# Optimization experiments

Measured on AMD Instinct MI355X. Metric: run time of the kernel, lower is better.

Reference implementation:

```python
import jax, jax.numpy as jnp
import numpy as np
import math

N, S, E, BS = 8, 8192, 256, 8


def setup_inputs() -> dict:
    key = jax.random.key(0)
    k1, k2, k3 = jax.random.split(key, 3)
    seq_vector = jax.random.normal(k1, (N, S, E), dtype=jnp.float32)
    # Conv1d weight [target_dim, source_dim] (kernel size 1 squeezed), default torch init scale
    bound = 1.0 / math.sqrt(E)
    W = jax.random.uniform(k2, (E, E), minval=-bound, maxval=bound, dtype=jnp.float32)
    sigma = math.sqrt(1.0 / (BS * E))
    bias = jax.random.uniform(k3, (BS,), minval=-sigma, maxval=sigma, dtype=jnp.float32)
    return {"seq_vector": seq_vector, "W": W, "bias": bias}


def reference(seq_vector, W, bias):
    n, s, e = seq_vector.shape
    bs = bias.shape[0]
    # 1x1 conv == per-token projection: [N,S,E] x [T,E] -> [N,S,T]
    features = jnp.einsum('nse,te->nst', seq_vector, W)
    # group sequence into blocks: [N, S//bs, bs, T]
    fb = features.reshape(n, s // bs, bs, -1)
    # blockwise causal (strictly lower-triangular) sum == exclusive cumsum over block dim
    excl = jnp.cumsum(fb, axis=2) - fb
    # position i gets bias[i]; position 0 additionally gets bias[0] a second time
    b_eff = bias.at[0].add(bias[0])  # [bs]
    out = excl + b_eff[None, None, :, None]
    return out.reshape(n, s, -1)
```

## Files before the change

### kernel.cpp

```cpp
#include <hip/hip_runtime.h>


typedef short short8 __attribute__((ext_vector_type(8)));
typedef float floatx4 __attribute__((ext_vector_type(4)));
typedef unsigned short ushort4v __attribute__((ext_vector_type(4)));

typedef const __attribute__((address_space(1))) unsigned int* gas_u32p;
typedef __attribute__((address_space(3))) unsigned int* las_u32p;

#define WAIT_VMCNT(n) __builtin_amdgcn_s_waitcnt(0x0F70 | ((n) & 0xF) | ((((n) >> 4) & 0x3) << 14))

__device__ __forceinline__ void gl2lds16(const void* g, void* l) {
    __builtin_amdgcn_global_load_lds((gas_u32p)g, (las_u32p)l, 16, 0, 0);
}

__device__ __forceinline__ unsigned short f2bf(float f) {
    union { float f; unsigned int u; } v;
    v.f = f;
    unsigned int u = v.u + 0x7fffu + ((v.u >> 16) & 1u);
    return (unsigned short)(u >> 16);
}

__device__ __forceinline__ short8 pack8(float4 f0, float4 f1) {
    short8 r;
    r[0] = (short)f2bf(f0.x); r[1] = (short)f2bf(f0.y);
    r[2] = (short)f2bf(f0.z); r[3] = (short)f2bf(f0.w);
    r[4] = (short)f2bf(f1.x); r[5] = (short)f2bf(f1.y);
    r[6] = (short)f2bf(f1.z); r[7] = (short)f2bf(f1.w);
    return r;
}

__global__ __launch_bounds__(256) void wconv_kernel(
    const float* __restrict__ W, unsigned short* __restrict__ Wb)
{
    const int i = (blockIdx.x * 256 + threadIdx.x) * 4;
    float4 f = *(const float4*)(W + i);
    ushort4v v;
    v[0] = f2bf(f.x); v[1] = f2bf(f.y); v[2] = f2bf(f.z); v[3] = f2bf(f.w);
    *(ushort4v*)(Wb + i) = v;
}

__global__ __launch_bounds__(512, 4) void bcl_gemm_kernel(
    const float* __restrict__ X, const unsigned short* __restrict__ Wb,
    const float* __restrict__ bias, float* __restrict__ out)
{
    __shared__ float buf[3][128 * 32];
    __shared__ unsigned short bW[64 * 256];

    const int tid  = threadIdx.x;
    const int lane = tid & 63;
    const int w    = tid >> 6;
    const int bx   = blockIdx.x;

    const int xcd = bx & 7;
    const int u   = bx >> 3;
    const int mg  = xcd * 64 + (u >> 2);
    const int ng  = u & 3;

    const int cl = lane & 15;
    const int q  = lane >> 4;

    const int srow = lane >> 3;
    const int sseg = (lane & 7) ^ srow;
    const float* gsrc0 = X + (size_t)(mg * 128 + w * 16 + srow) * 256 + sseg * 4;

#define STAGE(c, b)                                                            \
    do {                                                                       \
        const float* _g = gsrc0 + (c) * 32;                                    \
        _Pragma("unroll")                                                      \
        for (int _j = 0; _j < 2; ++_j)                                         \
            gl2lds16(_g + _j * 8 * 256, &buf[b][(w * 16 + _j * 8) * 32]);      \
    } while (0)

    {
        #pragma unroll
        for (int j = 0; j < 4; ++j) {
            const int n    = j * 16 + (tid >> 5);
            const int seg  = tid & 31;
            const int lseg = seg ^ (n & 15);
            const unsigned short* g =
                Wb + (size_t)(ng * 64 + n) * 256 + lseg * 8;
            gl2lds16(g, &bW[(size_t)(j * 512 + w * 64) * 8]);
        }
    }

    STAGE(0, 0);
    STAGE(1, 1);
    WAIT_VMCNT(4);
    __syncthreads();

    floatx4 acc[4];
    #pragma unroll
    for (int nt = 0; nt < 4; ++nt)
        acc[nt] = (floatx4){0.f, 0.f, 0.f, 0.f};

#define KSTEP(c, ALLOW)                                                        \
    do {                                                                       \
        if ((c) + 2 < 8) STAGE((c) + 2, ((c) + 2) % 3);                        \
        __builtin_amdgcn_sched_barrier(0);                                     \
        WAIT_VMCNT(ALLOW);                                                     \
        __builtin_amdgcn_sched_barrier(0);                                     \
        short8 Bf[4];                                                          \
        _Pragma("unroll")                                                      \
        for (int nt = 0; nt < 4; ++nt)                                         \
            Bf[nt] = *(const short8*)                                          \
                &bW[(nt * 16 + cl) * 256 + ((((c) * 4 + q) ^ cl) * 8)];        \
        float4 af[2];                                                          \
        _Pragma("unroll")                                                      \
        for (int h = 0; h < 2; ++h)                                            \
            af[h] = *(const float4*)                                           \
                &buf[(c) % 3][(w * 16 + cl) * 32 +                             \
                              ((((q << 1) | h) ^ (cl & 7)) << 2)];             \
        short8 a0 = pack8(af[0], af[1]);                                       \
        _Pragma("unroll")                                                      \
        for (int nt = 0; nt < 4; ++nt)                                         \
            acc[nt] = __builtin_amdgcn_mfma_f32_16x16x32_bf16(                 \
                a0, Bf[nt], acc[nt], 0, 0, 0);                                 \
    } while (0)

    KSTEP(0, 4);
    KSTEP(1, 4);
    KSTEP(2, 4);
    KSTEP(3, 4);
    KSTEP(4, 4);
    KSTEP(5, 4);
    KSTEP(6, 2);
    KSTEP(7, 0);
#undef KSTEP

    float be[4];
    {
        const int off = (q & 1) * 4;
        be[0] = bias[off + 0];
        be[1] = bias[off + 1];
        be[2] = bias[off + 2];
        be[3] = bias[off + 3];
        if (off == 0) be[0] += bias[0];
    }

    float* epi0 = &buf[0][(w * 16) * 32];
    float* epi1 = &buf[1][(w * 16) * 32];

    #pragma unroll
    for (int p = 0; p < 2; ++p) {
        float* epi = p ? epi1 : epi0;
        const bool act = ((q >> 1) == p);
        #pragma unroll
        for (int nt = 0; nt < 4; ++nt) {
            floatx4 v = acc[nt];
            float p1 = v[0];
            float p2 = p1 + v[1];
            float p3 = p2 + v[2];
            float tot = p3 + v[3];
            float below = __shfl_up(tot, 16);
            float p0 = 0.f;
            if (q & 1) { p0 = below; p1 += below; p2 += below; p3 += below; }
            if (act) {
                float* dst = epi + (q & 1) * 4 * 64 + nt * 16 + cl;
                dst[0]   = p0 + be[0];
                dst[64]  = p1 + be[1];
                dst[128] = p2 + be[2];
                dst[192] = p3 + be[3];
            }
        }
        #pragma unroll
        for (int k = 0; k < 2; ++k) {
            const int r   = k * 4 + (lane >> 4);
            const int c16 = lane & 15;
            floatx4 vv = *(const floatx4*)&epi[r * 64 + c16 * 4];
            const size_t grow = (size_t)(mg * 128 + w * 16 + p * 8 + r);
            *(floatx4*)&out[grow * 256 + ng * 64 + c16 * 4] = vv;
        }
    }
#undef STAGE
}

extern "C" void kernel_launch(void* const* d_in, const int* in_sizes, int n_in,
                              void* d_out, int out_size, void* d_ws, size_t ws_size,
                              hipStream_t stream)
{
    const float* X = (const float*)d_in[0];
    const float* W = (const float*)d_in[1];
    const float* B = (const float*)d_in[2];
    float* out = (float*)d_out;
    unsigned short* Wb = (unsigned short*)d_ws;

    wconv_kernel<<<dim3(64), dim3(256), 0, stream>>>(W, Wb);
    bcl_gemm_kernel<<<dim3(2048), dim3(512), 0, stream>>>(X, Wb, B, out);
}
```

Before: 141.4 us.

## Narrow N tile to 32 and stage A as bf16 via registers

```diff
diff --git a/kernel.cpp b/kernel.cpp
--- a/kernel.cpp
+++ b/kernel.cpp
@@ -2,6 +2,7 @@
 
 
 typedef short short8 __attribute__((ext_vector_type(8)));
+typedef short short4v __attribute__((ext_vector_type(4)));
 typedef float floatx4 __attribute__((ext_vector_type(4)));
 typedef unsigned short ushort4v __attribute__((ext_vector_type(4)));
 
@@ -21,12 +22,10 @@
     return (unsigned short)(u >> 16);
 }
 
-__device__ __forceinline__ short8 pack8(float4 f0, float4 f1) {
-    short8 r;
-    r[0] = (short)f2bf(f0.x); r[1] = (short)f2bf(f0.y);
-    r[2] = (short)f2bf(f0.z); r[3] = (short)f2bf(f0.w);
-    r[4] = (short)f2bf(f1.x); r[5] = (short)f2bf(f1.y);
-    r[6] = (short)f2bf(f1.z); r[7] = (short)f2bf(f1.w);
+__device__ __forceinline__ short4v pack4(float4 f) {
+    short4v r;
+    r[0] = (short)f2bf(f.x); r[1] = (short)f2bf(f.y);
+    r[2] = (short)f2bf(f.z); r[3] = (short)f2bf(f.w);
     return r;
 }
 
@@ -40,12 +39,12 @@
     *(ushort4v*)(Wb + i) = v;
 }
 
-__global__ __launch_bounds__(512, 4) void bcl_gemm_kernel(
+__global__ __launch_bounds__(512, 6) void bcl_gemm_kernel(
     const float* __restrict__ X, const unsigned short* __restrict__ Wb,
     const float* __restrict__ bias, float* __restrict__ out)
 {
-    __shared__ float buf[3][128 * 32];
-    __shared__ unsigned short bW[64 * 256];
+    __shared__ __align__(16) unsigned short aB[2][128 * 40];
+    __shared__ __align__(16) unsigned short bW[32 * 256];
 
     const int tid  = threadIdx.x;
     const int lane = tid & 63;
@@ -54,68 +53,72 @@
 
     const int xcd = bx & 7;
     const int u   = bx >> 3;
-    const int mg  = xcd * 64 + (u >> 2);
-    const int ng  = u & 3;
+    const int mg  = xcd * 64 + (u >> 3);
+    const int ng  = u & 7;
 
     const int cl = lane & 15;
     const int q  = lane >> 4;
 
     const int srow = lane >> 3;
-    const int sseg = (lane & 7) ^ srow;
-    const float* gsrc0 = X + (size_t)(mg * 128 + w * 16 + srow) * 256 + sseg * 4;
-
-#define STAGE(c, b)                                                            \
-    do {                                                                       \
-        const float* _g = gsrc0 + (c) * 32;                                    \
-        _Pragma("unroll")                                                      \
-        for (int _j = 0; _j < 2; ++_j)                                         \
-            gl2lds16(_g + _j * 8 * 256, &buf[b][(w * 16 + _j * 8) * 32]);      \
-    } while (0)
+    const float* gA = X + (size_t)(mg * 128 + w * 16 + srow) * 256 + (lane & 7) * 4;
 
     {
         #pragma unroll
-        for (int j = 0; j < 4; ++j) {
-            const int n    = j * 16 + (tid >> 5);
-            const int seg  = tid & 31;
+        for (int j = 0; j < 2; ++j) {
+            const int n    = j * 16 + w * 2 + (lane >> 5);
+            const int seg  = lane & 31;
             const int lseg = seg ^ (n & 15);
             const unsigned short* g =
-                Wb + (size_t)(ng * 64 + n) * 256 + lseg * 8;
+                Wb + (size_t)(ng * 32 + n) * 256 + lseg * 8;
             gl2lds16(g, &bW[(size_t)(j * 512 + w * 64) * 8]);
         }
     }
 
-    STAGE(0, 0);
-    STAGE(1, 1);
+    float4 sA[3][2];
+
+#define LOADA(c, s)                                                            \
+    do {                                                                       \
+        sA[s][0] = *(const float4*)(gA + (c) * 32);                            \
+        sA[s][1] = *(const float4*)(gA + (c) * 32 + 8 * 256);                  \
+    } while (0)
+
+#define WRITEA(c, s)                                                           \
+    do {                                                                       \
+        *(short4v*)&aB[(c) & 1][(w * 16 + srow) * 40 + (lane & 7) * 4] =       \
+            pack4(sA[s][0]);                                                   \
+        *(short4v*)&aB[(c) & 1][(w * 16 + srow + 8) * 40 + (lane & 7) * 4] =   \
+            pack4(sA[s][1]);                                                   \
+    } while (0)
+
+    LOADA(0, 0);
+    LOADA(1, 1);
+    LOADA(2, 2);
     WAIT_VMCNT(4);
+    WRITEA(0, 0);
     __syncthreads();
 
-    floatx4 acc[4];
-    #pragma unroll
-    for (int nt = 0; nt < 4; ++nt)
-        acc[nt] = (floatx4){0.f, 0.f, 0.f, 0.f};
+    floatx4 acc[2];
+    acc[0] = (floatx4){0.f, 0.f, 0.f, 0.f};
+    acc[1] = (floatx4){0.f, 0.f, 0.f, 0.f};
 
 #define KSTEP(c, ALLOW)                                                        \
     do {                                                                       \
-        if ((c) + 2 < 8) STAGE((c) + 2, ((c) + 2) % 3);                        \
+        if ((c) + 3 < 8) LOADA((c) + 3, ((c) + 3) % 3);                        \
+        short8 a0 = *(const short8*)                                           \
+            &aB[(c) & 1][(w * 16 + cl) * 40 + q * 8];                          \
+        short8 Bf0 = *(const short8*)                                          \
+            &bW[(0 * 16 + cl) * 256 + ((((c) * 4 + q) ^ cl) * 8)];             \
+        short8 Bf1 = *(const short8*)                                          \
+            &bW[(1 * 16 + cl) * 256 + ((((c) * 4 + q) ^ cl) * 8)];             \
+        if ((c) + 1 < 8) {                                                     \
+            WAIT_VMCNT(ALLOW);                                                 \
+            WRITEA((c) + 1, ((c) + 1) % 3);                                    \
+        }                                                                      \
+        acc[0] = __builtin_amdgcn_mfma_f32_16x16x32_bf16(a0, Bf0, acc[0],      \
+                                                         0, 0, 0);             \
+        acc[1] = __builtin_amdgcn_mfma_f32_16x16x32_bf16(a0, Bf1, acc[1],      \
+                                                         0, 0, 0);             \
         __builtin_amdgcn_sched_barrier(0);                                     \
-        WAIT_VMCNT(ALLOW);                                                     \
-        __builtin_amdgcn_sched_barrier(0);                                     \
-        short8 Bf[4];                                                          \
-        _Pragma("unroll")                                                      \
-        for (int nt = 0; nt < 4; ++nt)                                         \
-            Bf[nt] = *(const short8*)                                          \
-                &bW[(nt * 16 + cl) * 256 + ((((c) * 4 + q) ^ cl) * 8)];        \
-        float4 af[2];                                                          \
-        _Pragma("unroll")                                                      \
-        for (int h = 0; h < 2; ++h)                                            \
-            af[h] = *(const float4*)                                           \
-                &buf[(c) % 3][(w * 16 + cl) * 32 +                             \
-                              ((((q << 1) | h) ^ (cl & 7)) << 2)];             \
-        short8 a0 = pack8(af[0], af[1]);                                       \
-        _Pragma("unroll")                                                      \
-        for (int nt = 0; nt < 4; ++nt)                                         \
-            acc[nt] = __builtin_amdgcn_mfma_f32_16x16x32_bf16(                 \
-                a0, Bf[nt], acc[nt], 0, 0, 0);                                 \
     } while (0)
 
     KSTEP(0, 4);
@@ -123,8 +126,8 @@
     KSTEP(2, 4);
     KSTEP(3, 4);
     KSTEP(4, 4);
-    KSTEP(5, 4);
-    KSTEP(6, 2);
+    KSTEP(5, 2);
+    KSTEP(6, 0);
     KSTEP(7, 0);
 #undef KSTEP
 
@@ -138,15 +141,15 @@
         if (off == 0) be[0] += bias[0];
     }
 
-    float* epi0 = &buf[0][(w * 16) * 32];
-    float* epi1 = &buf[1][(w * 16) * 32];
+    float* epi0 = (float*)&aB[0][(w * 16) * 40];
+    float* epi1 = (float*)&aB[1][(w * 16) * 40];
 
     #pragma unroll
     for (int p = 0; p < 2; ++p) {
         float* epi = p ? epi1 : epi0;
         const bool act = ((q >> 1) == p);
         #pragma unroll
-        for (int nt = 0; nt < 4; ++nt) {
+        for (int nt = 0; nt < 2; ++nt) {
             floatx4 v = acc[nt];
             float p1 = v[0];
             float p2 = p1 + v[1];
@@ -156,23 +159,24 @@
             float p0 = 0.f;
             if (q & 1) { p0 = below; p1 += below; p2 += below; p3 += below; }
             if (act) {
-                float* dst = epi + (q & 1) * 4 * 64 + nt * 16 + cl;
-                dst[0]   = p0 + be[0];
-                dst[64]  = p1 + be[1];
-                dst[128] = p2 + be[2];
-                dst[192] = p3 + be[3];
+                float* dst = epi + (q & 1) * 4 * 32 + nt * 16 + cl;
+                dst[0]  = p0 + be[0];
+                dst[32] = p1 + be[1];
+                dst[64] = p2 + be[2];
+                dst[96] = p3 + be[3];
             }
         }
-        #pragma unroll
-        for (int k = 0; k < 2; ++k) {
-            const int r   = k * 4 + (lane >> 4);
-            const int c16 = lane & 15;
-            floatx4 vv = *(const floatx4*)&epi[r * 64 + c16 * 4];
+        {
+            const int r  = lane >> 3;
+            const int c8 = lane & 7;
+            floatx4 vv = *(const floatx4*)&epi[r * 32 + c8 * 4];
             const size_t grow = (size_t)(mg * 128 + w * 16 + p * 8 + r);
-            *(floatx4*)&out[grow * 256 + ng * 64 + c16 * 4] = vv;
+            *(floatx4*)&out[grow * 256 + ng * 32 + c8 * 4] = vv;
         }
     }
-#undef STAGE
+#undef LOADA
+#undef WRITEA
+
 }
 
 extern "C" void kernel_launch(void* const* d_in, const int* in_sizes, int n_in,
@@ -186,5 +190,5 @@
     unsigned short* Wb = (unsigned short*)d_ws;
 
     wconv_kernel<<<dim3(64), dim3(256), 0, stream>>>(W, Wb);
-    bcl_gemm_kernel<<<dim3(2048), dim3(512), 0, stream>>>(X, Wb, B, out);
+    bcl_gemm_kernel<<<dim3(4096), dim3(512), 0, stream>>>(X, Wb, B, out);
 }
```

New measurement: 153.9 us. +8.8%, slower.
